# Kernel optimization log

Hardware: AMD Instinct MI355X
Metric: run time of the kernel (lower is better)

Reference implementation:

```python
import jax, jax.numpy as jnp
import numpy as np

B, S, I, H, HI = 1024, 64, 2048, 2048, 2048  # batch, num_high_states, input_dim, hidden_dim, high_dim
L = 4          # num recurrent layers
NH = 16        # num heads
HD = H // NH   # head dim
MAX_STEPS = 100


def setup_inputs() -> dict:
    key = jax.random.key(0)
    ks = iter(jax.random.split(key, 40))
    std = 0.02
    d = {}
    d["x"] = jax.random.normal(next(ks), (B, I), jnp.float32)
    d["high_state"] = jax.random.normal(next(ks), (B, HI), jnp.float32)
    d["high_states_history"] = jax.random.normal(next(ks), (B, S, HI), jnp.float32)
    d["hidden"] = jax.random.normal(next(ks), (L, B, H), jnp.float32) * 0.1
    # input projection + timestep embedding
    d["W_in"] = jax.random.normal(next(ks), (I, H), jnp.float32) * std
    d["b_in"] = jnp.zeros((H,), jnp.float32)
    d["ts_emb"] = jax.random.normal(next(ks), (MAX_STEPS, H), jnp.float32) * std
    # hierarchical attention projections
    d["Wq"] = jax.random.normal(next(ks), (H, H), jnp.float32) * std
    d["bq"] = jnp.zeros((H,), jnp.float32)
    d["Wk"] = jax.random.normal(next(ks), (HI, H), jnp.float32) * std
    d["bk"] = jnp.zeros((H,), jnp.float32)
    d["Wv"] = jax.random.normal(next(ks), (HI, H), jnp.float32) * std
    d["bv"] = jnp.zeros((H,), jnp.float32)
    d["Wo"] = jax.random.normal(next(ks), (H, H), jnp.float32) * std
    d["bo"] = jnp.zeros((H,), jnp.float32)
    # per-layer GRU-like gates, stacked over layers; Linear in = I+H = 2H
    for nm in ("Wu", "Wr", "Ws", "Wc"):
        d[nm] = jax.random.normal(next(ks), (L, 2 * H, H), jnp.float32) * std
    for nm in ("bu", "br", "bs", "bc"):
        d[nm] = jnp.zeros((L, H), jnp.float32)
    # layer norm
    d["ln_g"] = jnp.ones((H,), jnp.float32)
    d["ln_b"] = jnp.zeros((H,), jnp.float32)
    d["timestep"] = 5
    return d


def _forward(x, high_states_history, hidden, W_in, b_in, ts_emb,
             Wq, bq, Wk, bk, Wv, bv, Wo, bo,
             Wu, bu, Wr, br, Ws, bs, Wc, bc, ln_g, ln_b, timestep):
    # input projection + timestep encoding
    x = x @ W_in + b_in + ts_emb[timestep]  # [B,H]
    # hierarchical attention (single query per batch element)
    q = (x @ Wq + bq).reshape(B, NH, HD)
    k = (high_states_history @ Wk + bk).reshape(B, S, NH, HD)
    v = (high_states_history @ Wv + bv).reshape(B, S, NH, HD)
    scores = jnp.einsum("bhd,bshd->bhs", q, k) / np.sqrt(HD).astype(np.float32)
    attn = jax.nn.softmax(scores, axis=-1)  # [B,NH,S]
    ctx = jnp.einsum("bhs,bshd->bhd", attn, v).reshape(B, H)
    x = x + (ctx @ Wo + bo)
    # stacked GRU-like recurrent layers (loop over fixed small L)
    new_hidden = []
    for i in range(L):
        h = hidden[i]
        comb = jnp.concatenate([x, h], axis=1)  # [B,2H]
        u = jax.nn.sigmoid(comb @ Wu[i] + bu[i])
        r = jax.nn.sigmoid(comb @ Wr[i] + br[i])
        s = jax.nn.sigmoid(comb @ Ws[i] + bs[i])
        comb_r = jnp.concatenate([x, r * h], axis=1)
        cand = jax.nn.gelu(comb_r @ Wc[i] + bc[i], approximate=False)
        new_h = (1 - u) * h + u * (s * cand + (1 - s) * h)
        new_hidden.append(new_h)
        x = new_h  # dropout is identity in eval
    # layer norm (eps matches torch default 1e-5)
    mu = jnp.mean(x, axis=-1, keepdims=True)
    var = jnp.mean(jnp.square(x - mu), axis=-1, keepdims=True)
    out = (x - mu) * jax.lax.rsqrt(var + 1e-5) * ln_g + ln_b
    return out, jnp.stack(new_hidden)


def reference(x, high_state, high_states_history, hidden, W_in, b_in, ts_emb,
              Wq, bq, Wk, bk, Wv, bv, Wo, bo,
              Wu, bu, Wr, br, Ws, bs, Wc, bc, ln_g, ln_b, timestep):
    # high_state is accepted by the original signature but unused in the body
    return _forward(x, high_states_history, hidden, W_in, b_in, ts_emb,
                    Wq, bq, Wk, bk, Wv, bv, Wo, bo,
                    Wu, bu, Wr, br, Ws, bs, Wc, bc, ln_g, ln_b, timestep)
```

## Files before the change

kernel.cpp:

```cpp
#include <hip/hip_runtime.h>
#include <hip/hip_bf16.h>
#include <math.h>

#define B_  1024
#define S_  64
#define H_  2048
#define L_  4
#define NH_ 16
#define HD_ 128
#define WSLAB_ ((size_t)2048 * 4096)

typedef __attribute__((ext_vector_type(4))) float floatx4;
typedef __attribute__((ext_vector_type(8))) short shortx8;

__device__ __forceinline__ unsigned short f2bf(float f) {
  union { float f; unsigned int u; } v; v.f = f;
  unsigned int u = v.u;
  return (unsigned short)((u + 0x7fffu + ((u >> 16) & 1u)) >> 16);
}

__device__ __forceinline__ void gload16(const void* g, void* l) {
  __builtin_amdgcn_global_load_lds(
      (const __attribute__((address_space(1))) void*)g,
      (__attribute__((address_space(3))) void*)l, 16, 0, 0);
}

__global__ __launch_bounds__(256) void preamble(
    const float* __restrict__ x, unsigned short* __restrict__ x_bf,
    const float* __restrict__ hidden, unsigned short* __restrict__ h_bf,
    const float* __restrict__ Wk, unsigned short* __restrict__ Wkb,
    const float* __restrict__ W_in, const float* __restrict__ Wq,
    const float* __restrict__ Wv, const float* __restrict__ Wo,
    unsigned short* __restrict__ WT4,
    const float* __restrict__ Wu, const float* __restrict__ Wr,
    const float* __restrict__ Ws, const float* __restrict__ Wc,
    unsigned short* __restrict__ TW0)
{
  __shared__ __align__(16) float smem[4160];
  const int t = threadIdx.x;
  const int g = blockIdx.x;
  if (g < 7168) {
    const float* in; unsigned short* out; int i;
    if (g < 1024)      { in = x;      out = x_bf; i = g * 256 + t; }
    else if (g < 5120) { in = hidden; out = h_bf; i = (g - 1024) * 256 + t; }
    else               { in = Wk;     out = Wkb;  i = (g - 5120) * 256 + t; }
    const float4* p = (const float4*)in;
    float4 a = p[i * 2], b = p[i * 2 + 1];
    unsigned short o[8] = { f2bf(a.x), f2bf(a.y), f2bf(a.z), f2bf(a.w),
                            f2bf(b.x), f2bf(b.y), f2bf(b.z), f2bf(b.w) };
    ((uint4*)out)[i] = *(uint4*)o;
    return;
  }
  float (*tile)[65] = (float(*)[65])smem;
  const float* src; unsigned short* outp; int K, k0, n0;
  if (g < 11264) {
    int bid = g - 7168;
    int z = bid >> 10, rem = bid & 1023;
    k0 = (rem >> 5) * 64; n0 = (rem & 31) * 64; K = 2048;
    src = (z == 0) ? W_in : (z == 1) ? Wq : (z == 2) ? Wv : Wo;
    outp = WT4 + (size_t)z * 2048 * 2048;
  } else {
    int bid = g - 11264;
    int z = bid >> 11, rem = bid & 2047;
    k0 = (rem >> 5) * 64; n0 = (rem & 31) * 64; K = 4096;
    src = (z == 0) ? Wu : (z == 1) ? Wr : (z == 2) ? Ws : Wc;
    outp = TW0 + (size_t)z * WSLAB_;
  }
  int tr = t >> 4, tc = (t & 15) * 4;
  #pragma unroll
  for (int rep = 0; rep < 4; ++rep) {
    int kk = tr + rep * 16;
    float4 v = *(const float4*)(src + (size_t)(k0 + kk) * 2048 + n0 + tc);
    tile[kk][tc] = v.x; tile[kk][tc + 1] = v.y;
    tile[kk][tc + 2] = v.z; tile[kk][tc + 3] = v.w;
  }
  __syncthreads();
  int nr = t >> 2, kc = (t & 3) * 16;
  unsigned short o[16];
  #pragma unroll
  for (int j = 0; j < 16; ++j) o[j] = f2bf(tile[kc + j][nr]);
  *(uint4*)(outp + (size_t)(n0 + nr) * K + k0 + kc)     = *(uint4*)&o[0];
  *(uint4*)(outp + (size_t)(n0 + nr) * K + k0 + kc + 8) = *(uint4*)&o[8];
}

enum { EPI_XIN = 0, EPI_QB = 1, EPI_X2 = 2, EPI_CTX = 3 };

template<int EPI>
__global__ __launch_bounds__(256, 2) void gemm32(
    const unsigned short* __restrict__ A0,
    const unsigned short* __restrict__ BT,
    const float* __restrict__ b0,
    const float* __restrict__ tse, const int* __restrict__ tsp,
    const float* __restrict__ res,
    float* __restrict__ Cf, unsigned short* __restrict__ Cb)
{
  const int t = threadIdx.x, wid = t >> 6, lane = t & 63, lr = lane & 15, lg = lane >> 4;
  const int g = blockIdx.x;
  const int m_base = (g >> 4) * 32;
  const int pn = g & 15;
  __shared__ unsigned short lds_a[32 * 64];
  __shared__ unsigned short lds_b[128 * 64];
  floatx4 acc[2][2] = {};
  const int arow = t >> 3, akc = t & 7;
  const int akcs = akc ^ (arow & 7);
  for (int kt = 0; kt < 32; ++kt) {
    {
      int gk = kt * 64 + akcs * 8;
      const unsigned short* ga;
      if (EPI == EPI_CTX) ga = A0 + ((size_t)(m_base + arow) * 16 + pn) * 2048 + gk;
      else                ga = A0 + (size_t)(m_base + arow) * 2048 + gk;
      gload16(ga, &lds_a[wid * 512]);
    }
    #pragma unroll
    for (int is = 0; is < 4; ++is) {
      int idx = is * 256 + t;
      int row = idx >> 3, kc = idx & 7;
      int kcs = kc ^ (row & 7);
      int gk = kt * 64 + kcs * 8;
      gload16(BT + (size_t)(pn * 128 + row) * 2048 + gk, &lds_b[(is * 256 + wid * 64) * 8]);
    }
    __syncthreads();
    #pragma unroll
    for (int ks = 0; ks < 2; ++ks) {
      const int cs = (((ks << 2) + lg) ^ (lr & 7)) * 8;
      shortx8 af[2], bfv[2];
      #pragma unroll
      for (int mt = 0; mt < 2; ++mt)
        af[mt] = *(shortx8*)&lds_a[(mt * 16 + lr) * 64 + cs];
      #pragma unroll
      for (int nt = 0; nt < 2; ++nt)
        bfv[nt] = *(shortx8*)&lds_b[(wid * 32 + nt * 16 + lr) * 64 + cs];
      #pragma unroll
      for (int mt = 0; mt < 2; ++mt)
        #pragma unroll
        for (int nt = 0; nt < 2; ++nt)
          acc[mt][nt] = __builtin_amdgcn_mfma_f32_16x16x32_bf16(af[mt], bfv[nt], acc[mt][nt], 0, 0, 0);
    }
    __syncthreads();
  }
  int ts = 0;
  if (EPI == EPI_XIN) ts = tsp[0];
  #pragma unroll
  for (int mt = 0; mt < 2; ++mt)
  #pragma unroll
  for (int nt = 0; nt < 2; ++nt)
  #pragma unroll
  for (int j = 0; j < 4; ++j) {
    int row = m_base + mt * 16 + lg * 4 + j;
    int col = pn * 128 + wid * 32 + nt * 16 + lr;
    size_t idx = (size_t)row * 2048 + col;
    float v = acc[mt][nt][j] + b0[col];
    if (EPI == EPI_XIN) {
      v += tse[(size_t)ts * 2048 + col];
      Cf[idx] = v; Cb[idx] = f2bf(v);
    } else if (EPI == EPI_QB) {
      Cb[idx] = f2bf(v);
    } else if (EPI == EPI_X2) {
      v += res[idx]; Cb[idx] = f2bf(v);
    } else {
      Cb[idx] = f2bf(v);
    }
  }
}

__global__ __launch_bounds__(256, 4) void gemm_gates(
    const unsigned short* __restrict__ Ax, const unsigned short* __restrict__ Ah,
    const unsigned short* __restrict__ TW,
    const float* __restrict__ bu, const float* __restrict__ br, const float* __restrict__ bs,
    const float* __restrict__ Hf,
    float* __restrict__ U, float* __restrict__ Sg,
    unsigned short* __restrict__ rh, float* __restrict__ Cc)
{
  const int t = threadIdx.x, wid = t >> 6, lane = t & 63, lr = lane & 15, lg = lane >> 4;
  const int wr = wid >> 1, wc = wid & 1;
  const int g = blockIdx.x;
  const int m_base = (g >> 6) * 64;
  const int pan = g & 63;
  const int n_base = (pan & 15) * 128;
  const int z = pan >> 4;
  const unsigned short* BTz = TW + (size_t)z * WSLAB_;
  __shared__ unsigned short lds_a[64 * 64];
  __shared__ unsigned short lds_b[128 * 64];
  floatx4 acc[2][4] = {};
  const int nkt = (z == 3) ? 32 : 64;
  for (int kt = 0; kt < nkt; ++kt) {
    #pragma unroll
    for (int is = 0; is < 2; ++is) {
      int idx = is * 256 + t;
      int row = idx >> 3, kc = idx & 7;
      int kcs = kc ^ (row & 7);
      int gk = kt * 64 + kcs * 8;
      const unsigned short* ga;
      if (z == 3 || gk < 2048) ga = Ax + (size_t)(m_base + row) * 2048 + gk;
      else                     ga = Ah + (size_t)(m_base + row) * 2048 + (gk - 2048);
      gload16(ga, &lds_a[(is * 256 + wid * 64) * 8]);
    }
    #pragma unroll
    for (int is = 0; is < 4; ++is) {
      int idx = is * 256 + t;
      int row = idx >> 3, kc = idx & 7;
      int kcs = kc ^ (row & 7);
      int gk = kt * 64 + kcs * 8;
      gload16(BTz + (size_t)(n_base + row) * 4096 + gk, &lds_b[(is * 256 + wid * 64) * 8]);
    }
    __syncthreads();
    #pragma unroll
    for (int ks = 0; ks < 2; ++ks) {
      const int cs = (((ks << 2) + lg) ^ (lr & 7)) * 8;
      shortx8 af[2], bfv[4];
      #pragma unroll
      for (int mt = 0; mt < 2; ++mt)
        af[mt] = *(shortx8*)&lds_a[(wr * 32 + mt * 16 + lr) * 64 + cs];
      #pragma unroll
      for (int nt = 0; nt < 4; ++nt)
        bfv[nt] = *(shortx8*)&lds_b[(wc * 64 + nt * 16 + lr) * 64 + cs];
      #pragma unroll
      for (int mt = 0; mt < 2; ++mt)
        #pragma unroll
        for (int nt = 0; nt < 4; ++nt)
          acc[mt][nt] = __builtin_amdgcn_mfma_f32_16x16x32_bf16(af[mt], bfv[nt], acc[mt][nt], 0, 0, 0);
    }
    __syncthreads();
  }
  #pragma unroll
  for (int mt = 0; mt < 2; ++mt)
  #pragma unroll
  for (int nt = 0; nt < 4; ++nt)
  #pragma unroll
  for (int j = 0; j < 4; ++j) {
    int row = m_base + wr * 32 + mt * 16 + lg * 4 + j;
    int col = n_base + wc * 64 + nt * 16 + lr;
    size_t idx = (size_t)row * 2048 + col;
    float v = acc[mt][nt][j];
    if (z == 0)      U[idx]  = 1.f / (1.f + expf(-(v + bu[col])));
    else if (z == 1) rh[idx] = f2bf((1.f / (1.f + expf(-(v + br[col])))) * Hf[idx]);
    else if (z == 2) Sg[idx] = 1.f / (1.f + expf(-(v + bs[col])));
    else             Cc[idx] = v;
  }
}

__global__ __launch_bounds__(256) void cand_tconv(
    const unsigned short* __restrict__ Arh, const unsigned short* __restrict__ TW,
    const float* __restrict__ bc, const float* __restrict__ Cc,
    const float* __restrict__ U, const float* __restrict__ Sg,
    const float* __restrict__ Hf,
    float* __restrict__ nh_f, unsigned short* __restrict__ nh_b,
    const float* __restrict__ Wun, const float* __restrict__ Wrn,
    const float* __restrict__ Wsn, const float* __restrict__ Wcn,
    unsigned short* __restrict__ TWnext)
{
  __shared__ __align__(16) float smem[5120];
  const int t = threadIdx.x;
  if (blockIdx.x < 512) {
    unsigned short* lds_a = (unsigned short*)smem;
    unsigned short* lds_b = (unsigned short*)smem + 2048;
    const int wid = t >> 6, lane = t & 63, lr = lane & 15, lg = lane >> 4;
    const int g = blockIdx.x;
    const int m_base = (g >> 4) * 32;
    const int pn = g & 15;
    const unsigned short* BTz = TW + (size_t)3 * WSLAB_;
    floatx4 acc[2][2] = {};
    const int arow = t >> 3, akc = t & 7;
    const int akcs = akc ^ (arow & 7);
    for (int kt = 0; kt < 32; ++kt) {
      gload16(Arh + (size_t)(m_base + arow) * 2048 + kt * 64 + akcs * 8, &lds_a[wid * 512]);
      #pragma unroll
      for (int is = 0; is < 4; ++is) {
        int idx = is * 256 + t;
        int row = idx >> 3, kc = idx & 7;
        int kcs = kc ^ (row & 7);
        int gk = kt * 64 + kcs * 8;
        gload16(BTz + (size_t)(pn * 128 + row) * 4096 + 2048 + gk, &lds_b[(is * 256 + wid * 64) * 8]);
      }
      __syncthreads();
      #pragma unroll
      for (int ks = 0; ks < 2; ++ks) {
        const int cs = (((ks << 2) + lg) ^ (lr & 7)) * 8;
        shortx8 af[2], bfv[2];
        #pragma unroll
        for (int mt = 0; mt < 2; ++mt)
          af[mt] = *(shortx8*)&lds_a[(mt * 16 + lr) * 64 + cs];
        #pragma unroll
        for (int nt = 0; nt < 2; ++nt)
          bfv[nt] = *(shortx8*)&lds_b[(wid * 32 + nt * 16 + lr) * 64 + cs];
        #pragma unroll
        for (int mt = 0; mt < 2; ++mt)
          #pragma unroll
          for (int nt = 0; nt < 2; ++nt)
            acc[mt][nt] = __builtin_amdgcn_mfma_f32_16x16x32_bf16(af[mt], bfv[nt], acc[mt][nt], 0, 0, 0);
      }
      __syncthreads();
    }
    #pragma unroll
    for (int mt = 0; mt < 2; ++mt)
    #pragma unroll
    for (int nt = 0; nt < 2; ++nt)
    #pragma unroll
    for (int j = 0; j < 4; ++j) {
      int row = m_base + mt * 16 + lg * 4 + j;
      int col = pn * 128 + wid * 32 + nt * 16 + lr;
      size_t idx = (size_t)row * 2048 + col;
      float v = acc[mt][nt][j] + Cc[idx] + bc[col];
      float gl = 0.5f * v * (1.f + erff(v * 0.70710678118654752f));
      float u = U[idx], s = Sg[idx], hh = Hf[idx];
      float nh = (1.f - u) * hh + u * (s * gl + (1.f - s) * hh);
      nh_f[idx] = nh; nh_b[idx] = f2bf(nh);
    }
  } else {
    if (TWnext == nullptr) return;
    float (*tile)[65] = (float(*)[65])smem;
    int bid = blockIdx.x - 512;
    int z = bid >> 11;
    int rem = bid & 2047;
    int k0 = (rem >> 5) * 64;
    int n0 = (rem & 31) * 64;
    const float* src = (z == 0) ? Wun : (z == 1) ? Wrn : (z == 2) ? Wsn : Wcn;
    unsigned short* outp = TWnext + (size_t)z * WSLAB_;
    int tr = t >> 4, tc = (t & 15) * 4;
    #pragma unroll
    for (int rep = 0; rep < 4; ++rep) {
      int kk = tr + rep * 16;
      float4 v = *(const float4*)(src + (size_t)(k0 + kk) * 2048 + n0 + tc);
      tile[kk][tc] = v.x; tile[kk][tc + 1] = v.y;
      tile[kk][tc + 2] = v.z; tile[kk][tc + 3] = v.w;
    }
    __syncthreads();
    int nr = t >> 2, kc = (t & 3) * 16;
    unsigned short o[16];
    #pragma unroll
    for (int j = 0; j < 16; ++j) o[j] = f2bf(tile[kc + j][nr]);
    *(uint4*)(outp + (size_t)(n0 + nr) * 4096 + k0 + kc)     = *(uint4*)&o[0];
    *(uint4*)(outp + (size_t)(n0 + nr) * 4096 + k0 + kc + 8) = *(uint4*)&o[8];
  }
}

__global__ __launch_bounds__(256) void gemm_t(
    const unsigned short* __restrict__ Q, const unsigned short* __restrict__ Wk,
    unsigned short* __restrict__ T)
{
  const int t = threadIdx.x, wid = t >> 6, lane = t & 63, lr = lane & 15, lg = lane >> 4;
  const int wr = wid >> 1, wc = wid & 1;
  const int h = blockIdx.z, m_base = blockIdx.x * 64, n_base = blockIdx.y * 128;
  __shared__ unsigned short lds_a[64 * 32], lds_b[128 * 32];
  floatx4 acc[2][4] = {};
  const int arow = t >> 2, akc = t & 3;
  const int akcs = akc ^ ((arow >> 1) & 3);
  for (int kt = 0; kt < 4; ++kt) {
    gload16(Q + (size_t)(m_base + arow) * 2048 + h * 128 + kt * 32 + akcs * 8,
            &lds_a[wid * 512]);
    #pragma unroll
    for (int is = 0; is < 2; ++is) {
      int idx = is * 256 + t;
      int row = idx >> 2, kc = idx & 3;
      int kcs = kc ^ ((row >> 1) & 3);
      gload16(Wk + (size_t)(n_base + row) * 2048 + h * 128 + kt * 32 + kcs * 8,
              &lds_b[(is * 256 + wid * 64) * 8]);
    }
    __syncthreads();
    const int sl = lg ^ ((lr >> 1) & 3);
    shortx8 af[2], bfv[4];
    #pragma unroll
    for (int mt = 0; mt < 2; ++mt)
      af[mt] = *(shortx8*)&lds_a[(wr * 32 + mt * 16 + lr) * 32 + sl * 8];
    #pragma unroll
    for (int nt = 0; nt < 4; ++nt)
      bfv[nt] = *(shortx8*)&lds_b[(wc * 64 + nt * 16 + lr) * 32 + sl * 8];
    #pragma unroll
    for (int mt = 0; mt < 2; ++mt)
      #pragma unroll
      for (int nt = 0; nt < 4; ++nt)
        acc[mt][nt] = __builtin_amdgcn_mfma_f32_16x16x32_bf16(af[mt], bfv[nt], acc[mt][nt], 0, 0, 0);
    __syncthreads();
  }
  #pragma unroll
  for (int mt = 0; mt < 2; ++mt)
  #pragma unroll
  for (int nt = 0; nt < 4; ++nt)
  #pragma unroll
  for (int j = 0; j < 4; ++j) {
    int row_o = m_base + wr * 32 + mt * 16 + lg * 4 + j;
    int col   = n_base + wc * 64 + nt * 16 + lr;
    T[((size_t)row_o * 16 + h) * 2048 + col] = f2bf(acc[mt][nt][j]);
  }
}

__global__ __launch_bounds__(256) void attn_fused(
    const unsigned short* __restrict__ T, const float* __restrict__ hist,
    unsigned short* __restrict__ Wb)
{
  const int t = threadIdx.x;
  const int wid = t >> 6, lane = t & 63, lr = lane & 15, lg = lane >> 4;
  const int b = blockIdx.x;
  __shared__ unsigned short lds_t[16 * 72];
  __shared__ unsigned short lds_h[64 * 72];
  __shared__ float sc[16 * 68];
  __shared__ float ps[64 * 16];
  floatx4 acc = {};
  for (int kt = 0; kt < 32; ++kt) {
    { int row = t >> 4, c4 = t & 15;
      int k = kt * 64 + c4 * 4;
      ushort4 v = *(const ushort4*)(T + ((size_t)b * 16 + row) * 2048 + k);
      *(ushort4*)&lds_t[row * 72 + c4 * 4] = v; }
    #pragma unroll
    for (int rep = 0; rep < 4; ++rep) {
      int idx = t + rep * 256;
      int srow = idx >> 4, c4 = idx & 15;
      int k = kt * 64 + c4 * 4;
      float4 hv = *(const float4*)(hist + ((size_t)b * 64 + srow) * 2048 + k);
      ushort4 uv; uv.x = f2bf(hv.x); uv.y = f2bf(hv.y); uv.z = f2bf(hv.z); uv.w = f2bf(hv.w);
      *(ushort4*)&lds_h[srow * 72 + c4 * 4] = uv;
    }
    __syncthreads();
    #pragma unroll
    for (int ks = 0; ks < 2; ++ks) {
      shortx8 af = *(shortx8*)&lds_t[lr * 72 + ks * 32 + lg * 8];
      shortx8 bv = *(shortx8*)&lds_h[(wid * 16 + lr) * 72 + ks * 32 + lg * 8];
      acc = __builtin_amdgcn_mfma_f32_16x16x32_bf16(af, bv, acc, 0, 0, 0);
    }
    __syncthreads();
  }
  #pragma unroll
  for (int j = 0; j < 4; ++j)
    sc[(lg * 4 + j) * 68 + wid * 16 + lr] = acc[j] * 0.088388347648318447f;
  __syncthreads();
  if (t < 64) {
    int h = t >> 2, qd = t & 3;
    float vv[16];
    float m = -1e30f;
    #pragma unroll
    for (int zz = 0; zz < 16; ++zz) { vv[zz] = sc[h * 68 + qd * 16 + zz]; m = fmaxf(m, vv[zz]); }
    m = fmaxf(m, __shfl_xor(m, 1)); m = fmaxf(m, __shfl_xor(m, 2));
    float sum = 0.f;
    #pragma unroll
    for (int zz = 0; zz < 16; ++zz) { vv[zz] = expf(vv[zz] - m); sum += vv[zz]; }
    sum += __shfl_xor(sum, 1); sum += __shfl_xor(sum, 2);
    float inv = 1.f / sum;
    #pragma unroll
    for (int zz = 0; zz < 16; ++zz)
      ps[(qd * 16 + zz) * 16 + h] = vv[zz] * inv;
  }
  __syncthreads();
  const int i0 = t * 8;
  floatx4 wacc[16][2] = {};
  const floatx4* ps4 = (const floatx4*)ps;
  for (int s = 0; s < 64; ++s) {
    const float* hp = hist + ((size_t)b * 64 + s) * 2048 + i0;
    float4 h4a = *(const float4*)hp;
    float4 h4b = *(const float4*)(hp + 4);
    floatx4 hva = { h4a.x, h4a.y, h4a.z, h4a.w };
    floatx4 hvb = { h4b.x, h4b.y, h4b.z, h4b.w };
    #pragma unroll
    for (int hq = 0; hq < 4; ++hq) {
      floatx4 p = ps4[s * 4 + hq];
      wacc[hq * 4 + 0][0] += p.x * hva; wacc[hq * 4 + 0][1] += p.x * hvb;
      wacc[hq * 4 + 1][0] += p.y * hva; wacc[hq * 4 + 1][1] += p.y * hvb;
      wacc[hq * 4 + 2][0] += p.z * hva; wacc[hq * 4 + 2][1] += p.z * hvb;
      wacc[hq * 4 + 3][0] += p.w * hva; wacc[hq * 4 + 3][1] += p.w * hvb;
    }
  }
  #pragma unroll
  for (int h = 0; h < 16; ++h) {
    unsigned short o[8];
    #pragma unroll
    for (int j = 0; j < 4; ++j) { o[j] = f2bf(wacc[h][0][j]); o[4 + j] = f2bf(wacc[h][1][j]); }
    *(uint4*)(Wb + ((size_t)b * 16 + h) * 2048 + i0) = *(uint4*)o;
  }
}

__global__ __launch_bounds__(256) void lnorm(
    const float* __restrict__ X, const float* __restrict__ gma,
    const float* __restrict__ bta, float* __restrict__ out)
{
  const int row = blockIdx.x, t = threadIdx.x;
  float4 a = *(const float4*)(X + (size_t)row * 2048 + t * 4);
  float4 c = *(const float4*)(X + (size_t)row * 2048 + 1024 + t * 4);
  float sum = a.x + a.y + a.z + a.w + c.x + c.y + c.z + c.w;
  float sq = a.x*a.x + a.y*a.y + a.z*a.z + a.w*a.w + c.x*c.x + c.y*c.y + c.z*c.z + c.w*c.w;
  #pragma unroll
  for (int off = 1; off < 64; off <<= 1) {
    sum += __shfl_xor(sum, off);
    sq  += __shfl_xor(sq, off);
  }
  __shared__ float red[8];
  int wid = t >> 6, lane = t & 63;
  if (lane == 0) { red[wid] = sum; red[wid + 4] = sq; }
  __syncthreads();
  sum = red[0] + red[1] + red[2] + red[3];
  sq  = red[4] + red[5] + red[6] + red[7];
  float mu = sum * (1.f / 2048.f);
  float var = sq * (1.f / 2048.f) - mu * mu;
  float rs = rsqrtf(var + 1e-5f);
  const float* pa = &a.x; const float* pc = &c.x;
  #pragma unroll
  for (int j = 0; j < 4; ++j) {
    int col = t * 4 + j;
    out[(size_t)row * 2048 + col] = (pa[j] - mu) * rs * gma[col] + bta[col];
  }
  #pragma unroll
  for (int j = 0; j < 4; ++j) {
    int col = 1024 + t * 4 + j;
    out[(size_t)row * 2048 + col] = (pc[j] - mu) * rs * gma[col] + bta[col];
  }
}

extern "C" void kernel_launch(void* const* d_in, const int* in_sizes, int n_in,
                              void* d_out, int out_size, void* d_ws, size_t ws_size,
                              hipStream_t stream) {
  (void)in_sizes; (void)n_in; (void)out_size; (void)ws_size;
  const float* x      = (const float*)d_in[0];
  const float* hist   = (const float*)d_in[2];
  const float* hidden = (const float*)d_in[3];
  const float* W_in   = (const float*)d_in[4];
  const float* b_in   = (const float*)d_in[5];
  const float* ts_emb = (const float*)d_in[6];
  const float* Wq     = (const float*)d_in[7];
  const float* bq     = (const float*)d_in[8];
  const float* Wk     = (const float*)d_in[9];
  const float* Wv     = (const float*)d_in[11];
  const float* bv     = (const float*)d_in[12];
  const float* Wo     = (const float*)d_in[13];
  const float* bo     = (const float*)d_in[14];
  const float* Wu     = (const float*)d_in[15];
  const float* Wr     = (const float*)d_in[16];
  const float* Wsg    = (const float*)d_in[17];
  const float* Wc     = (const float*)d_in[18];
  const float* bu     = (const float*)d_in[19];
  const float* br     = (const float*)d_in[20];
  const float* bs     = (const float*)d_in[21];
  const float* bc     = (const float*)d_in[22];
  const float* ln_g   = (const float*)d_in[23];
  const float* ln_b   = (const float*)d_in[24];
  const int*   tsp    = (const int*)d_in[25];
  float* out = (float*)d_out;

  const size_t BH = (size_t)B_ * H_;
  char* w = (char*)d_ws;
  auto take = [&](size_t bytes) { char* p = w; w += bytes; return p; };

  unsigned short* TW0  = (unsigned short*)take((size_t)4 * WSLAB_ * 2);
  unsigned short* TW1  = (unsigned short*)take((size_t)4 * WSLAB_ * 2);
  unsigned short* Tb   = (unsigned short*)take((size_t)B_ * 16 * 2048 * 2);
  unsigned short* WT4  = (unsigned short*)take((size_t)4 * H_ * H_ * 2);
  unsigned short* WinT = WT4;
  unsigned short* WqT  = WT4 + (size_t)H_ * H_;
  unsigned short* WvT  = WT4 + (size_t)2 * H_ * H_;
  unsigned short* WoT  = WT4 + (size_t)3 * H_ * H_;
  unsigned short* Wkb  = (unsigned short*)take((size_t)H_ * H_ * 2);
  unsigned short* x_bf   = (unsigned short*)take(BH * 2);
  unsigned short* h_bf   = (unsigned short*)take((size_t)L_ * BH * 2);
  unsigned short* xin_bf = (unsigned short*)take(BH * 2);
  unsigned short* q_bf   = (unsigned short*)take(BH * 2);
  unsigned short* ctx_bf = (unsigned short*)take(BH * 2);
  unsigned short* x2_bf  = (unsigned short*)take(BH * 2);
  unsigned short* rh_bf  = (unsigned short*)take(BH * 2);
  unsigned short* xa     = (unsigned short*)take(BH * 2);
  unsigned short* xb     = (unsigned short*)take(BH * 2);
  float* U   = (float*)take(BH * 4);
  float* Sg  = (float*)take(BH * 4);
  float* Cc  = (float*)take(BH * 4);
  float* XIN = out;

  dim3 blk(256);

  preamble<<<dim3(19456), blk, 0, stream>>>(
      x, x_bf, hidden, h_bf, Wk, Wkb,
      W_in, Wq, Wv, Wo, WT4,
      Wu, Wr, Wsg, Wc, TW0);

  gemm32<EPI_XIN><<<dim3(512), blk, 0, stream>>>(
      x_bf, WinT, b_in, ts_emb, tsp, nullptr, XIN, xin_bf);
  gemm32<EPI_QB><<<dim3(512), blk, 0, stream>>>(
      xin_bf, WqT, bq, nullptr, nullptr, nullptr, nullptr, q_bf);
  gemm_t<<<dim3(16, 16, 16), blk, 0, stream>>>(q_bf, Wkb, Tb);
  attn_fused<<<dim3(1024), blk, 0, stream>>>(Tb, hist, Tb);
  gemm32<EPI_CTX><<<dim3(512), blk, 0, stream>>>(
      Tb, WvT, bv, nullptr, nullptr, nullptr, nullptr, ctx_bf);
  gemm32<EPI_X2><<<dim3(512), blk, 0, stream>>>(
      ctx_bf, WoT, bo, nullptr, nullptr, XIN, nullptr, x2_bf);

  unsigned short* xcur = x2_bf;
  for (int i = 0; i < L_; ++i) {
    const float* h_i = hidden + (size_t)i * BH;
    float* nh_f = out + BH + (size_t)i * BH;
    unsigned short* nh_b = (i & 1) ? xb : xa;
    unsigned short* TWcur = (i & 1) ? TW1 : TW0;
    unsigned short* TWnxt = (i < 3) ? ((i & 1) ? TW0 : TW1) : nullptr;
    gemm_gates<<<dim3(1024), blk, 0, stream>>>(
        xcur, h_bf + (size_t)i * BH, TWcur,
        bu + (size_t)i * H_, br + (size_t)i * H_, bs + (size_t)i * H_,
        h_i, U, Sg, rh_bf, Cc);
    int grid = (i < 3) ? 8704 : 512;
    size_t off = (size_t)(i + 1) * WSLAB_;
    cand_tconv<<<dim3(grid), blk, 0, stream>>>(
        rh_bf, TWcur, bc + (size_t)i * H_, Cc, U, Sg, h_i, nh_f, nh_b,
        Wu + off, Wr + off, Wsg + off, Wc + off, TWnxt);
    xcur = nh_b;
  }

  lnorm<<<dim3(1024), blk, 0, stream>>>(out + BH + (size_t)3 * BH, ln_g, ln_b, out);
}
```

Measured before the change: 1.089 ms.

## Stream history once through LDS with online softmax in attention kernel

Restructures the fused attention kernel so each block loads the high-state history in chunks of 8 rows. Each chunk is converted to bf16 into swizzled LDS and reused for both the score MFMA and the probability-weighted sum. Softmax becomes an online running max and sum, with rescaling of the accumulators per chunk and final normalization. This removes the second full fp32 read of the large history tensor from global memory. In exchange it uses bf16-rounded history in the weighted sum, adds more syncthreads per chunk, and uses larger LDS that may lower occupancy.

```diff
diff --git a/kernel.cpp b/kernel.cpp
--- a/kernel.cpp
+++ b/kernel.cpp
@@ -384,85 +384,120 @@
   }
 }
 
-__global__ __launch_bounds__(256) void attn_fused(
+__global__ __launch_bounds__(256) void attn_once(
     const unsigned short* __restrict__ T, const float* __restrict__ hist,
     unsigned short* __restrict__ Wb)
 {
   const int t = threadIdx.x;
   const int wid = t >> 6, lane = t & 63, lr = lane & 15, lg = lane >> 4;
   const int b = blockIdx.x;
-  __shared__ unsigned short lds_t[16 * 72];
-  __shared__ unsigned short lds_h[64 * 72];
-  __shared__ float sc[16 * 68];
-  __shared__ float ps[64 * 16];
-  floatx4 acc = {};
-  for (int kt = 0; kt < 32; ++kt) {
-    { int row = t >> 4, c4 = t & 15;
-      int k = kt * 64 + c4 * 4;
-      ushort4 v = *(const ushort4*)(T + ((size_t)b * 16 + row) * 2048 + k);
-      *(ushort4*)&lds_t[row * 72 + c4 * 4] = v; }
-    #pragma unroll
-    for (int rep = 0; rep < 4; ++rep) {
-      int idx = t + rep * 256;
-      int srow = idx >> 4, c4 = idx & 15;
-      int k = kt * 64 + c4 * 4;
-      float4 hv = *(const float4*)(hist + ((size_t)b * 64 + srow) * 2048 + k);
-      ushort4 uv; uv.x = f2bf(hv.x); uv.y = f2bf(hv.y); uv.z = f2bf(hv.z); uv.w = f2bf(hv.w);
-      *(ushort4*)&lds_h[srow * 72 + c4 * 4] = uv;
-    }
-    __syncthreads();
-    #pragma unroll
-    for (int ks = 0; ks < 2; ++ks) {
-      shortx8 af = *(shortx8*)&lds_t[lr * 72 + ks * 32 + lg * 8];
-      shortx8 bv = *(shortx8*)&lds_h[(wid * 16 + lr) * 72 + ks * 32 + lg * 8];
-      acc = __builtin_amdgcn_mfma_f32_16x16x32_bf16(af, bv, acc, 0, 0, 0);
-    }
-    __syncthreads();
-  }
-  #pragma unroll
-  for (int j = 0; j < 4; ++j)
-    sc[(lg * 4 + j) * 68 + wid * 16 + lr] = acc[j] * 0.088388347648318447f;
+  __shared__ unsigned short lds_h[8 * 2048];
+  __shared__ unsigned short lds_t[4 * 1024];
+  __shared__ float red[4][64][4];
+  __shared__ float sc[16][16];
+  __shared__ float ps[8][16];
+  __shared__ float mh[16], lh[16], fh[16];
+  if (t < 16) { mh[t] = -1e30f; lh[t] = 0.f; }
+  floatx4 wacc[16][2] = {};
+  const int i0 = t * 8;
+  for (int c = 0; c < 8; ++c) {
+    __syncthreads();
+    #pragma unroll
+    for (int is = 0; is < 8; ++is) {
+      int ic = is * 256 + t;
+      int row = ic >> 8, pos = ic & 255;
+      const float* hp = hist + ((size_t)b * 64 + c * 8 + row) * 2048 + pos * 8;
+      float4 a = *(const float4*)hp;
+      float4 bb = *(const float4*)(hp + 4);
+      unsigned short o[8] = { f2bf(a.x), f2bf(a.y), f2bf(a.z), f2bf(a.w),
+                              f2bf(bb.x), f2bf(bb.y), f2bf(bb.z), f2bf(bb.w) };
+      *(uint4*)&lds_h[(row * 256 + (pos ^ row)) * 8] = *(uint4*)o;
+    }
+    __syncthreads();
+    floatx4 acc = {};
+    for (int kk = 0; kk < 8; ++kk) {
+      int kt = wid * 8 + kk;
+      {
+        int r0 = lane >> 3, c0 = lane & 7;
+        gload16(T + ((size_t)b * 16 + r0) * 2048 + kt * 64 + (c0 ^ (r0 & 7)) * 8,
+                &lds_t[wid * 1024]);
+        int r1 = 8 + r0;
+        gload16(T + ((size_t)b * 16 + r1) * 2048 + kt * 64 + (c0 ^ (r1 & 7)) * 8,
+                &lds_t[wid * 1024 + 512]);
+      }
+      asm volatile("s_waitcnt vmcnt(0)" ::: "memory");
+      #pragma unroll
+      for (int ks = 0; ks < 2; ++ks) {
+        shortx8 af = *(shortx8*)&lds_t[wid * 1024 + (lr * 8 + ((ks * 4 + lg) ^ (lr & 7))) * 8];
+        int hr = lr & 7;
+        shortx8 bv = *(shortx8*)&lds_h[(hr * 256 + ((kt * 8 + ks * 4 + lg) ^ hr)) * 8];
+        acc = __builtin_amdgcn_mfma_f32_16x16x32_bf16(af, bv, acc, 0, 0, 0);
+      }
+    }
+    #pragma unroll
+    for (int j = 0; j < 4; ++j) red[wid][lane][j] = acc[j];
+    __syncthreads();
+    {
+      int h = t >> 4, sp = t & 15;
+      int rl = ((h >> 2) << 4) | sp;
+      int j = h & 3;
+      float v = red[0][rl][j] + red[1][rl][j] + red[2][rl][j] + red[3][rl][j];
+      sc[h][sp] = v * 0.088388347648318447f;
+    }
+    __syncthreads();
+    if (t < 16) {
+      float pm = sc[t][0];
+      #pragma unroll
+      for (int s2 = 1; s2 < 8; ++s2) pm = fmaxf(pm, sc[t][s2]);
+      float mn = fmaxf(mh[t], pm);
+      float f = expf(mh[t] - mn);
+      float sum = 0.f;
+      #pragma unroll
+      for (int s2 = 0; s2 < 8; ++s2) {
+        float p = expf(sc[t][s2] - mn);
+        ps[s2][t] = p; sum += p;
+      }
+      lh[t] = lh[t] * f + sum;
+      mh[t] = mn; fh[t] = f;
+    }
+    __syncthreads();
+    #pragma unroll
+    for (int h = 0; h < 16; ++h) {
+      float f = fh[h];
+      wacc[h][0] *= f; wacc[h][1] *= f;
+    }
+    #pragma unroll
+    for (int s2 = 0; s2 < 8; ++s2) {
+      uint4 hv = *(uint4*)&lds_h[((s2 * 256) + (t ^ s2)) * 8];
+      unsigned short hu[8]; *(uint4*)hu = hv;
+      float he[8];
+      #pragma unroll
+      for (int e = 0; e < 8; ++e) {
+        unsigned int u = (unsigned int)hu[e] << 16;
+        union { unsigned int u; float f; } cv; cv.u = u; he[e] = cv.f;
+      }
+      floatx4 hva = { he[0], he[1], he[2], he[3] };
+      floatx4 hvb = { he[4], he[5], he[6], he[7] };
+      #pragma unroll
+      for (int hq = 0; hq < 4; ++hq) {
+        floatx4 p4 = *(floatx4*)&ps[s2][hq * 4];
+        wacc[hq * 4 + 0][0] += p4.x * hva; wacc[hq * 4 + 0][1] += p4.x * hvb;
+        wacc[hq * 4 + 1][0] += p4.y * hva; wacc[hq * 4 + 1][1] += p4.y * hvb;
+        wacc[hq * 4 + 2][0] += p4.z * hva; wacc[hq * 4 + 2][1] += p4.z * hvb;
+        wacc[hq * 4 + 3][0] += p4.w * hva; wacc[hq * 4 + 3][1] += p4.w * hvb;
+      }
+    }
+  }
   __syncthreads();
-  if (t < 64) {
-    int h = t >> 2, qd = t & 3;
-    float vv[16];
-    float m = -1e30f;
-    #pragma unroll
-    for (int zz = 0; zz < 16; ++zz) { vv[zz] = sc[h * 68 + qd * 16 + zz]; m = fmaxf(m, vv[zz]); }
-    m = fmaxf(m, __shfl_xor(m, 1)); m = fmaxf(m, __shfl_xor(m, 2));
-    float sum = 0.f;
-    #pragma unroll
-    for (int zz = 0; zz < 16; ++zz) { vv[zz] = expf(vv[zz] - m); sum += vv[zz]; }
-    sum += __shfl_xor(sum, 1); sum += __shfl_xor(sum, 2);
-    float inv = 1.f / sum;
-    #pragma unroll
-    for (int zz = 0; zz < 16; ++zz)
-      ps[(qd * 16 + zz) * 16 + h] = vv[zz] * inv;
-  }
-  __syncthreads();
-  const int i0 = t * 8;
-  floatx4 wacc[16][2] = {};
-  const floatx4* ps4 = (const floatx4*)ps;
-  for (int s = 0; s < 64; ++s) {
-    const float* hp = hist + ((size_t)b * 64 + s) * 2048 + i0;
-    float4 h4a = *(const float4*)hp;
-    float4 h4b = *(const float4*)(hp + 4);
-    floatx4 hva = { h4a.x, h4a.y, h4a.z, h4a.w };
-    floatx4 hvb = { h4b.x, h4b.y, h4b.z, h4b.w };
-    #pragma unroll
-    for (int hq = 0; hq < 4; ++hq) {
-      floatx4 p = ps4[s * 4 + hq];
-      wacc[hq * 4 + 0][0] += p.x * hva; wacc[hq * 4 + 0][1] += p.x * hvb;
-      wacc[hq * 4 + 1][0] += p.y * hva; wacc[hq * 4 + 1][1] += p.y * hvb;
-      wacc[hq * 4 + 2][0] += p.z * hva; wacc[hq * 4 + 2][1] += p.z * hvb;
-      wacc[hq * 4 + 3][0] += p.w * hva; wacc[hq * 4 + 3][1] += p.w * hvb;
-    }
-  }
   #pragma unroll
   for (int h = 0; h < 16; ++h) {
+    float linv = 1.f / lh[h];
     unsigned short o[8];
     #pragma unroll
-    for (int j = 0; j < 4; ++j) { o[j] = f2bf(wacc[h][0][j]); o[4 + j] = f2bf(wacc[h][1][j]); }
+    for (int j = 0; j < 4; ++j) {
+      o[j]     = f2bf(wacc[h][0][j] * linv);
+      o[4 + j] = f2bf(wacc[h][1][j] * linv);
+    }
     *(uint4*)(Wb + ((size_t)b * 16 + h) * 2048 + i0) = *(uint4*)o;
   }
 }
@@ -572,7 +607,7 @@
   gemm32<EPI_QB><<<dim3(512), blk, 0, stream>>>(
       xin_bf, WqT, bq, nullptr, nullptr, nullptr, nullptr, q_bf);
   gemm_t<<<dim3(16, 16, 16), blk, 0, stream>>>(q_bf, Wkb, Tb);
-  attn_fused<<<dim3(1024), blk, 0, stream>>>(Tb, hist, Tb);
+  attn_once<<<dim3(1024), blk, 0, stream>>>(Tb, hist, Tb);
   gemm32<EPI_CTX><<<dim3(512), blk, 0, stream>>>(
       Tb, WvT, bv, nullptr, nullptr, nullptr, nullptr, ctx_bf);
   gemm32<EPI_X2><<<dim3(512), blk, 0, stream>>>(
```

New measurement: 1.181 ms. 8.4% more time.
